# Optimization experiments

Measured on AMD Instinct MI355X. Metric: run time of the kernel, lower is better.

Reference implementation:

```python
import jax, jax.numpy as jnp
import numpy as np

D_MODEL = 1024
N_HEADS = 16
D_HEAD = D_MODEL // N_HEADS
WINDOW = 256
SCALE = D_HEAD ** -0.5


def setup_inputs() -> dict:
    key = jax.random.key(0)
    ks = jax.random.split(key, 5)
    B, S = 2, 2048
    x = jax.random.normal(ks[0], (B, S, D_MODEL), dtype=jnp.float32)
    # weights stored as [d_in, d_out] so forward is x @ W + b
    W_qkv = jax.random.normal(ks[1], (D_MODEL, 3 * D_MODEL), dtype=jnp.float32) * (D_MODEL ** -0.5)
    b_qkv = jnp.zeros((3 * D_MODEL,), dtype=jnp.float32)
    W_out = jax.random.normal(ks[2], (D_MODEL, D_MODEL), dtype=jnp.float32) * (D_MODEL ** -0.5)
    b_out = jnp.zeros((D_MODEL,), dtype=jnp.float32)
    return {"x": x, "W_qkv": W_qkv, "b_qkv": b_qkv, "W_out": W_out, "b_out": b_out}


def _window_mask(S):
    # Faithful to source: keep positions where (i <= j) & (i >= j - WINDOW + 1),
    # i = query index (rows), j = key index (cols). (Anti-causal window, as in repo.)
    idx = jnp.arange(S)
    keep = (idx[:, None] <= idx[None, :]) & (idx[:, None] >= idx[None, :] - WINDOW + 1)
    return keep  # [S, S] bool


def reference(x, W_qkv, b_qkv, W_out, b_out):
    B, S, D = x.shape
    qkv = x @ W_qkv + b_qkv                      # [B,S,3D]
    q, k, v = jnp.split(qkv, 3, axis=-1)
    def heads(t):
        return t.reshape(B, S, N_HEADS, D_HEAD).transpose(0, 2, 1, 3)  # [B,H,S,dh]
    q, k, v = heads(q), heads(k), heads(v)
    attn = jnp.einsum('bhid,bhjd->bhij', q, k) * SCALE  # [B,H,S,S]
    keep = _window_mask(S)
    attn = jnp.where(keep[None, None], attn, -jnp.inf)
    attn = jax.nn.softmax(attn, axis=-1)
    # dropout is identity in eval mode
    out = jnp.einsum('bhij,bhjd->bhid', attn, v)        # [B,H,S,dh]
    out = out.transpose(0, 2, 1, 3).reshape(B, S, D)
    return out @ W_out + b_out
```

## Files before the change

### kernel.cpp

```cpp
#include <hip/hip_runtime.h>

typedef __bf16 bf16x8 __attribute__((ext_vector_type(8)));
typedef float f32x4 __attribute__((ext_vector_type(4)));
typedef unsigned short u16x8 __attribute__((ext_vector_type(8)));
typedef unsigned short u16x4 __attribute__((ext_vector_type(4)));

#define MFMA16(a, b, c) __builtin_amdgcn_mfma_f32_16x16x32_bf16((a), (b), (c), 0, 0, 0)

__device__ __forceinline__ unsigned short f2bf(float f) {
  union { float f; unsigned int i; } v; v.f = f;
  unsigned int u = v.i;
  u += 0x7fffu + ((u >> 16) & 1u);
  return (unsigned short)(u >> 16);
}

__device__ __forceinline__ void gload16(const void* g, void* l) {
  __builtin_amdgcn_global_load_lds(
      (const __attribute__((address_space(1))) unsigned int*)g,
      (__attribute__((address_space(3))) unsigned int*)l, 16, 0, 0);
}

__global__ __launch_bounds__(256) void convert_x(const float* __restrict__ X,
                                                 unsigned short* __restrict__ Xb) {
  size_t i = (size_t)(blockIdx.x * 256 + threadIdx.x) * 8;
  f32x4 f0 = *(const f32x4*)(X + i);
  f32x4 f1 = *(const f32x4*)(X + i + 4);
  u16x8 t;
#pragma unroll
  for (int j = 0; j < 4; ++j) { t[j] = f2bf(f0[j]); t[4 + j] = f2bf(f1[j]); }
  *(u16x8*)(Xb + i) = t;
}

__global__ __launch_bounds__(256) void transpose_w(const float* __restrict__ W,
                                                   unsigned short* __restrict__ Wt,
                                                   int N) {
  __shared__ unsigned short t[32][33];
  int tx = threadIdx.x & 31, ty = threadIdx.x >> 5;
  int bx = blockIdx.x;
  int by = blockIdx.y;
#pragma unroll
  for (int j = 0; j < 4; ++j) {
    int r = ty + j * 8;
    t[tx][r] = f2bf(W[(size_t)(by * 32 + r) * N + bx * 32 + tx]);
  }
  __syncthreads();
#pragma unroll
  for (int j = 0; j < 4; ++j) {
    int r = ty + j * 8;
    Wt[(size_t)(bx * 32 + r) * 1024 + by * 32 + tx] = t[r][tx];
  }
}

__global__ __launch_bounds__(256) void gemm_bt(
    const unsigned short* __restrict__ A, const unsigned short* __restrict__ Bt,
    const float* __restrict__ bias,
    unsigned short* __restrict__ O0, unsigned short* __restrict__ O1,
    unsigned short* __restrict__ O2, float* __restrict__ OF, int mode) {
  __shared__ __align__(16) unsigned short As[128 * 32];
  __shared__ __align__(16) unsigned short Bs[128 * 32];

  const int K = 1024;
  int tid = threadIdx.x;
  int lane = tid & 63, wave = tid >> 6, quad = lane >> 4, l16 = lane & 15;
  int wrow = wave >> 1, wcol = wave & 1;
  int m0 = blockIdx.x * 128, n0 = blockIdx.y * 128;

  const unsigned short* ag[2]; const unsigned short* bg[2];
  char* al[2]; char* bl[2];
#pragma unroll
  for (int i = 0; i < 2; ++i) {
    int c = tid + 256 * i, row = c >> 2, u = c & 3;
    ag[i] = A + (size_t)(m0 + row) * K + u * 8;
    bg[i] = Bt + (size_t)(n0 + row) * K + u * 8;
    al[i] = (char*)As + c * 16;
    bl[i] = (char*)Bs + c * 16;
  }

  int abase = (wrow * 64 + l16) * 64 + quad * 16;
  int bbase = (wcol * 64 + l16) * 64 + quad * 16;

  f32x4 acc[4][4];
#pragma unroll
  for (int i = 0; i < 4; ++i)
#pragma unroll
    for (int j = 0; j < 4; ++j) acc[i][j] = f32x4{0.f, 0.f, 0.f, 0.f};

  for (int k0 = 0; k0 < K; k0 += 32) {
#pragma unroll
    for (int i = 0; i < 2; ++i) {
      gload16(ag[i] + k0, al[i]);
      gload16(bg[i] + k0, bl[i]);
    }
    __syncthreads();
    bf16x8 af[4], bfr[4];
#pragma unroll
    for (int t = 0; t < 4; ++t) {
      af[t]  = *(const bf16x8*)((const char*)As + abase + t * 1024);
      bfr[t] = *(const bf16x8*)((const char*)Bs + bbase + t * 1024);
    }
#pragma unroll
    for (int mt = 0; mt < 4; ++mt)
#pragma unroll
      for (int nt = 0; nt < 4; ++nt)
        acc[mt][nt] = MFMA16(af[mt], bfr[nt], acc[mt][nt]);
    __syncthreads();
  }

  if (mode == 0) {
#pragma unroll
    for (int nt = 0; nt < 4; ++nt) {
      int n = n0 + wcol * 64 + nt * 16 + l16;
      float bv = bias[n];
      int seg = n >> 10, cc = n & 1023, hh = cc >> 6, d = cc & 63;
#pragma unroll
      for (int mt = 0; mt < 4; ++mt) {
        int mb = m0 + wrow * 64 + mt * 16 + quad * 4;
        int b = mb >> 11, s = mb & 2047;
        if (seg == 2) {
          u16x4 pk;
#pragma unroll
          for (int r = 0; r < 4; ++r) pk[r] = f2bf(acc[mt][nt][r] + bv);
          *(u16x4*)&O2[((size_t)((b << 4) + hh) * 64 + d) * 2048 + s] = pk;
        } else {
          unsigned short* O = seg ? O1 : O0;
#pragma unroll
          for (int r = 0; r < 4; ++r)
            O[((size_t)((b << 4) + hh) * 2048 + (s + r)) * 64 + d] = f2bf(acc[mt][nt][r] + bv);
        }
      }
    }
  } else {
#pragma unroll
    for (int nt = 0; nt < 4; ++nt) {
      int n = n0 + wcol * 64 + nt * 16 + l16;
      float bv = bias[n];
#pragma unroll
      for (int mt = 0; mt < 4; ++mt) {
        int mb = m0 + wrow * 64 + mt * 16 + quad * 4;
#pragma unroll
        for (int r = 0; r < 4; ++r)
          OF[(size_t)(mb + r) * 1024 + n] = acc[mt][nt][r] + bv;
      }
    }
  }
}

__global__ __launch_bounds__(256) void attn_kernel(
    const unsigned short* __restrict__ Q, const unsigned short* __restrict__ Kq,
    const unsigned short* __restrict__ Vt, unsigned short* __restrict__ AO) {
  __shared__ __align__(16) unsigned short Ks[32][72];
  __shared__ __align__(16) unsigned short Vs[64][40];
  __shared__ __align__(16) unsigned short Ps[4][16][40];

  int bid = blockIdx.x;
  int qblk = bid & 31, h = (bid >> 5) & 15, b = bid >> 9;
  int q0 = qblk * 64;
  int tid = threadIdx.x, lane = tid & 63, wave = tid >> 6, quad = lane >> 4, l16 = lane & 15;

  const unsigned short* Qb = Q + (size_t)(((b << 4) + h) * 2048) * 64;
  const unsigned short* Kb = Kq + (size_t)(((b << 4) + h) * 2048) * 64;
  const unsigned short* Vb = Vt + (size_t)(((b << 4) + h) * 64) * 2048;

  int qrow = q0 + wave * 16 + l16;
  bf16x8 qf0 = __builtin_bit_cast(bf16x8, *(const u16x8*)&Qb[(size_t)qrow * 64 + quad * 8]);
  bf16x8 qf1 = __builtin_bit_cast(bf16x8, *(const u16x8*)&Qb[(size_t)qrow * 64 + 32 + quad * 8]);

  float mrow[4], lrow[4];
  f32x4 zero = {0.f, 0.f, 0.f, 0.f};
  f32x4 o[4];
#pragma unroll
  for (int i = 0; i < 4; ++i) o[i] = zero;
#pragma unroll
  for (int r = 0; r < 4; ++r) { mrow[r] = -1e30f; lrow[r] = 0.f; }

  const float SCALE = 0.125f;
  int pstart = (wave >= 2) ? 1 : 0;
  int pend = pstart + 8;

  int ki = tid >> 3, kc = (tid & 7) * 8;
  int vd = tid >> 2, vc = (tid & 3) * 8;

  for (int p = 0; p < 10; ++p) {
    int kbase = q0 + p * 32;
    {
      int s = kbase + ki; s = s > 2047 ? 2047 : s;
      *(u16x8*)&Ks[ki][kc] = *(const u16x8*)&Kb[(size_t)s * 64 + kc];
    }
    if (kbase + vc + 7 <= 2047) {
      *(u16x8*)&Vs[vd][vc] = *(const u16x8*)&Vb[(size_t)vd * 2048 + kbase + vc];
    } else {
#pragma unroll
      for (int j = 0; j < 8; ++j) {
        int s = kbase + vc + j; s = s > 2047 ? 2047 : s;
        Vs[vd][vc + j] = Vb[(size_t)vd * 2048 + s];
      }
    }
    __syncthreads();

    if (p >= pstart && p <= pend) {
      f32x4 sc[2];
#pragma unroll
      for (int t = 0; t < 2; ++t) {
        bf16x8 kf0 = __builtin_bit_cast(bf16x8, *(const u16x8*)&Ks[t * 16 + l16][quad * 8]);
        bf16x8 kf1 = __builtin_bit_cast(bf16x8, *(const u16x8*)&Ks[t * 16 + l16][32 + quad * 8]);
        f32x4 z = zero;
        z = MFMA16(qf0, kf0, z);
        z = MFMA16(qf1, kf1, z);
        sc[t] = z;
      }
      float sv[2][4];
#pragma unroll
      for (int t = 0; t < 2; ++t)
#pragma unroll
        for (int r = 0; r < 4; ++r) {
          int kg = kbase + t * 16 + l16;
          int qg = q0 + wave * 16 + quad * 4 + r;
          bool valid = (kg >= qg) && (kg <= qg + 255) && (kg < 2048);
          sv[t][r] = valid ? sc[t][r] * SCALE : -1e30f;
        }
#pragma unroll
      for (int r = 0; r < 4; ++r) {
        float v = fmaxf(sv[0][r], sv[1][r]);
        v = fmaxf(v, __shfl_xor(v, 1));
        v = fmaxf(v, __shfl_xor(v, 2));
        v = fmaxf(v, __shfl_xor(v, 4));
        v = fmaxf(v, __shfl_xor(v, 8));
        float mnew = fmaxf(mrow[r], v);
        float alpha = __expf(mrow[r] - mnew);
        mrow[r] = mnew;
        float p0 = __expf(sv[0][r] - mnew);
        float p1 = __expf(sv[1][r] - mnew);
        p0 = (sv[0][r] > -5e29f) ? p0 : 0.f;
        p1 = (sv[1][r] > -5e29f) ? p1 : 0.f;
        float rs = p0 + p1;
        rs += __shfl_xor(rs, 1);
        rs += __shfl_xor(rs, 2);
        rs += __shfl_xor(rs, 4);
        rs += __shfl_xor(rs, 8);
        lrow[r] = lrow[r] * alpha + rs;
#pragma unroll
        for (int nt = 0; nt < 4; ++nt) o[nt][r] *= alpha;
        Ps[wave][quad * 4 + r][l16] = f2bf(p0);
        Ps[wave][quad * 4 + r][16 + l16] = f2bf(p1);
      }
      __threadfence_block();
      bf16x8 pf = __builtin_bit_cast(bf16x8, *(const u16x8*)&Ps[wave][l16][quad * 8]);
#pragma unroll
      for (int nt = 0; nt < 4; ++nt) {
        bf16x8 vf = __builtin_bit_cast(bf16x8, *(const u16x8*)&Vs[nt * 16 + l16][quad * 8]);
        o[nt] = MFMA16(pf, vf, o[nt]);
      }
    }
    __syncthreads();
  }

  unsigned short* dst = AO + ((size_t)(b * 2048 + q0 + wave * 16) * 1024) + h * 64;
#pragma unroll
  for (int nt = 0; nt < 4; ++nt)
#pragma unroll
    for (int r = 0; r < 4; ++r) {
      int qq = quad * 4 + r;
      dst[(size_t)qq * 1024 + nt * 16 + l16] = f2bf(o[nt][r] / lrow[r]);
    }
}

extern "C" void kernel_launch(void* const* d_in, const int* in_sizes, int n_in,
                              void* d_out, int out_size, void* d_ws, size_t ws_size,
                              hipStream_t stream) {
  const float* x = (const float*)d_in[0];
  const float* W_qkv = (const float*)d_in[1];
  const float* b_qkv = (const float*)d_in[2];
  const float* W_out = (const float*)d_in[3];
  const float* b_out = (const float*)d_in[4];
  float* out = (float*)d_out;

  unsigned short* ws = (unsigned short*)d_ws;
  unsigned short* Qw  = ws;
  unsigned short* Kw  = ws + 4194304;
  unsigned short* Vw  = ws + 8388608;
  unsigned short* Wqt = ws + 12582912;
  unsigned short* AO  = ws + 12582912;
  unsigned short* Wot = ws;
  unsigned short* Xb  = (unsigned short*)d_out;

  dim3 blk(256);
  convert_x<<<dim3(2048), blk, 0, stream>>>(x, Xb);
  transpose_w<<<dim3(96, 32), blk, 0, stream>>>(W_qkv, Wqt, 3072);
  gemm_bt<<<dim3(32, 24), blk, 0, stream>>>(Xb, Wqt, b_qkv, Qw, Kw, Vw, nullptr, 0);
  attn_kernel<<<dim3(1024), blk, 0, stream>>>(Qw, Kw, Vw, AO);
  transpose_w<<<dim3(32, 32), blk, 0, stream>>>(W_out, Wot, 1024);
  gemm_bt<<<dim3(32, 8), blk, 0, stream>>>(AO, Wot, b_out, nullptr, nullptr, nullptr, out, 1);
}
```

Before: 187.5 us.

## Double-buffer GEMM LDS tiles with async global-to-LDS prefetch and swizzle blocks

Adds a second LDS buffer so the global_load_lds for the next K-slice is issued before computing the current one, using vmcnt waits and raw barriers instead of full syncthreads. This targets load latency that was exposed on every K iteration. It also remaps workgroup IDs with an 8-way swizzle to improve L2 reuse of A/B tiles. LDS use doubles, which may reduce occupancy, and correctness depends on hand-written waitcnt ordering.

```diff
diff --git a/kernel.cpp b/kernel.cpp
--- a/kernel.cpp
+++ b/kernel.cpp
@@ -56,24 +56,30 @@
     const float* __restrict__ bias,
     unsigned short* __restrict__ O0, unsigned short* __restrict__ O1,
     unsigned short* __restrict__ O2, float* __restrict__ OF, int mode) {
-  __shared__ __align__(16) unsigned short As[128 * 32];
-  __shared__ __align__(16) unsigned short Bs[128 * 32];
+  __shared__ __align__(16) unsigned short As0[128 * 32];
+  __shared__ __align__(16) unsigned short Bs0[128 * 32];
+  __shared__ __align__(16) unsigned short As1[128 * 32];
+  __shared__ __align__(16) unsigned short Bs1[128 * 32];
 
   const int K = 1024;
   int tid = threadIdx.x;
   int lane = tid & 63, wave = tid >> 6, quad = lane >> 4, l16 = lane & 15;
   int wrow = wave >> 1, wcol = wave & 1;
-  int m0 = blockIdx.x * 128, n0 = blockIdx.y * 128;
+
+  int gx = gridDim.x;
+  int nwg = gx * gridDim.y;
+  int lin = blockIdx.y * gx + blockIdx.x;
+  int swz = (lin & 7) * (nwg >> 3) + (lin >> 3);
+  int m0 = (swz % gx) * 128, n0 = (swz / gx) * 128;
 
   const unsigned short* ag[2]; const unsigned short* bg[2];
-  char* al[2]; char* bl[2];
+  int loff[2];
 #pragma unroll
   for (int i = 0; i < 2; ++i) {
     int c = tid + 256 * i, row = c >> 2, u = c & 3;
     ag[i] = A + (size_t)(m0 + row) * K + u * 8;
     bg[i] = Bt + (size_t)(n0 + row) * K + u * 8;
-    al[i] = (char*)As + c * 16;
-    bl[i] = (char*)Bs + c * 16;
+    loff[i] = c * 16;
   }
 
   int abase = (wrow * 64 + l16) * 64 + quad * 16;
@@ -85,26 +91,48 @@
 #pragma unroll
     for (int j = 0; j < 4; ++j) acc[i][j] = f32x4{0.f, 0.f, 0.f, 0.f};
 
-  for (int k0 = 0; k0 < K; k0 += 32) {
+  auto STAGE = [&](int k0, char* Asb, char* Bsb) {
 #pragma unroll
     for (int i = 0; i < 2; ++i) {
-      gload16(ag[i] + k0, al[i]);
-      gload16(bg[i] + k0, bl[i]);
-    }
-    __syncthreads();
+      gload16(ag[i] + k0, Asb + loff[i]);
+      gload16(bg[i] + k0, Bsb + loff[i]);
+    }
+  };
+  auto COMPUTE = [&](const char* Asb, const char* Bsb) {
     bf16x8 af[4], bfr[4];
 #pragma unroll
     for (int t = 0; t < 4; ++t) {
-      af[t]  = *(const bf16x8*)((const char*)As + abase + t * 1024);
-      bfr[t] = *(const bf16x8*)((const char*)Bs + bbase + t * 1024);
+      af[t]  = *(const bf16x8*)(Asb + abase + t * 1024);
+      bfr[t] = *(const bf16x8*)(Bsb + bbase + t * 1024);
     }
 #pragma unroll
     for (int mt = 0; mt < 4; ++mt)
 #pragma unroll
       for (int nt = 0; nt < 4; ++nt)
         acc[mt][nt] = MFMA16(af[mt], bfr[nt], acc[mt][nt]);
-    __syncthreads();
-  }
+  };
+#define WAIT_VM4  asm volatile("s_waitcnt vmcnt(4)" ::: "memory")
+#define WAIT_VM0  asm volatile("s_waitcnt vmcnt(0)" ::: "memory")
+#define WAIT_LGKM asm volatile("s_waitcnt lgkmcnt(0)" ::: "memory")
+#define BAR       __builtin_amdgcn_s_barrier()
+
+  STAGE(0, (char*)As0, (char*)Bs0);
+  for (int t = 0; t < 30; t += 2) {
+    STAGE((t + 1) * 32, (char*)As1, (char*)Bs1);
+    WAIT_VM4; BAR;
+    COMPUTE((const char*)As0, (const char*)Bs0);
+    WAIT_LGKM; BAR;
+    STAGE((t + 2) * 32, (char*)As0, (char*)Bs0);
+    WAIT_VM4; BAR;
+    COMPUTE((const char*)As1, (const char*)Bs1);
+    WAIT_LGKM; BAR;
+  }
+  STAGE(31 * 32, (char*)As1, (char*)Bs1);
+  WAIT_VM4; BAR;
+  COMPUTE((const char*)As0, (const char*)Bs0);
+  WAIT_LGKM; BAR;
+  WAIT_VM0; BAR;
+  COMPUTE((const char*)As1, (const char*)Bs1);
 
   if (mode == 0) {
 #pragma unroll
```

Result: faster. 176.6 us (-5.8%).
